# Optimization experiments

Hardware: AMD Instinct MI355X
Metric: run time of the kernel (lower is better)

The kernel has to match this reference:

```python
import jax, jax.numpy as jnp
import numpy as np

B, H, W, P = 2, 224, 224, 256


def setup_inputs() -> dict:
    key = jax.random.key(0)
    ks = jax.random.split(key, 7)
    x = jax.random.normal(ks[0], (B, 1, H, W), dtype=jnp.float32)
    offset_x1 = jax.random.uniform(ks[1], (P,), jnp.float32, -16.0, 16.0)
    offset_x2 = jax.random.uniform(ks[2], (P,), jnp.float32, -16.0, 16.0)
    offset_y1 = jax.random.uniform(ks[3], (P,), jnp.float32, -16.0, 16.0)
    offset_y2 = jax.random.uniform(ks[4], (P,), jnp.float32, -16.0, 16.0)
    radii = jax.random.randint(ks[5], (P,), 1, 4).astype(jnp.int32)  # {1,2,3}
    thresholds = jax.random.normal(ks[6], (P,), dtype=jnp.float32) * 0.1
    return {
        'x': x,
        'offset_x1': offset_x1, 'offset_x2': offset_x2,
        'offset_y1': offset_y1, 'offset_y2': offset_y2,
        'radii': radii, 'thresholds': thresholds,
        'max_radius': 3,
    }


def reference(x, offset_x1, offset_x2, offset_y1, offset_y2, radii, thresholds, max_radius):
    Bb, _, Hh, Ww = x.shape
    r = int(max_radius)
    dtype = x.dtype
    # replicate-padded integral image, zero-padded by 1 on top/left -> [B, Hp+1, Wp+1]
    xp = jnp.pad(x, ((0, 0), (0, 0), (r, r), (r, r)), mode='edge')
    integral = jnp.cumsum(jnp.cumsum(xp, axis=2), axis=3)
    integral = jnp.pad(integral, ((0, 0), (0, 0), (1, 0), (1, 0)))[:, 0]

    base_y = jnp.arange(Hh, dtype=dtype)[None, :, None]   # [1,H,1]
    base_x = jnp.arange(Ww, dtype=dtype)[None, None, :]   # [1,1,W]
    rad = radii.astype(jnp.int32)[:, None, None]           # [P,1,1]
    area = ((2.0 * radii.astype(dtype) + 1.0) ** 2)[:, None, None]

    def box_mean(off_y, off_x):
        # clamped float centers, truncated to int (non-negative -> trunc == floor)
        cy = jnp.clip(base_y + off_y[:, None, None], 0.0, Hh - 1).astype(jnp.int32) + r
        cx = jnp.clip(base_x + off_x[:, None, None], 0.0, Ww - 1).astype(jnp.int32) + r
        y0, x0 = cy - rad, cx - rad
        y1, x1 = cy + rad + 1, cx + rad + 1
        g = lambda yi, xi: integral[:, yi, xi]  # gather -> [B,P,H,W]
        s = g(y1, x1) - g(y0, x1) - g(y1, x0) + g(y0, x0)
        return s / area

    diff = box_mean(offset_y1, offset_x1) - box_mean(offset_y2, offset_x2)
    # binarize=False: return centered differences
    return diff - thresholds[None, :, None, None].astype(diff.dtype)
```

## Files before the change

kernel.cpp:

```cpp
#include <hip/hip_runtime.h>

#define BN 2
#define HN 224
#define WN 224
#define PN 256
#define RN 3
#define IW 231
#define ISZ (IW * IW)
#define NPIX (HN * WN)

__global__ __launch_bounds__(256) void integral_rows_kernel(
    const float* __restrict__ x, float* __restrict__ I)
{
    const int wave = (blockIdx.x * 256 + threadIdx.x) >> 6;
    const int lane = threadIdx.x & 63;
    if (wave >= BN * IW) return;
    const int b = wave / IW, i = wave % IW;
    float* Ib = I + b * ISZ + i * IW;
    if (i == 0) {
        for (int j = lane; j < IW; j += 64) Ib[j] = 0.0f;
        return;
    }
    int yy = i - 1 - RN;
    yy = yy < 0 ? 0 : (yy > HN - 1 ? HN - 1 : yy);
    const float* xr = x + b * HN * WN + yy * WN;

    float carry = 0.0f;
#pragma unroll
    for (int c = 0; c < 4; ++c) {
        const int j = c * 64 + lane;
        float v = 0.0f;
        if (j >= 1 && j < IW) {
            int xx = j - 1 - RN;
            xx = xx < 0 ? 0 : (xx > WN - 1 ? WN - 1 : xx);
            v = xr[xx];
        }
#pragma unroll
        for (int d = 1; d < 64; d <<= 1) {
            float n = __shfl_up(v, d, 64);
            if (lane >= d) v += n;
        }
        v += carry;
        if (j < IW) Ib[j] = v;
        carry = __shfl(v, 63, 64);
    }
}

__global__ __launch_bounds__(256) void integral_cols_kernel(float* __restrict__ I)
{
    const int t = blockIdx.x * 256 + threadIdx.x;
    if (t >= BN * IW) return;
    const int b = t / IW, j = t % IW;
    float* Ib = I + b * ISZ;
    float acc = 0.0f;
#pragma unroll 11
    for (int i = 1; i < IW; ++i) {
        acc += Ib[i * IW + j];
        Ib[i * IW + j] = acc;
    }
}

__global__ __launch_bounds__(256) void box_mean_kernel(
    const float* __restrict__ I, float* __restrict__ BM)
{
    const int xt = blockIdx.x;
    const int zb = blockIdx.z;
    const int r_idx = zb >> 1, b = zb & 1;
    const int rad = r_idx + 1;
    const float inv_area = 1.0f / (float)((2 * rad + 1) * (2 * rad + 1));
    const int x = xt * 64 + threadIdx.x;
    const int xc = x < WN ? x : WN - 1;
    const int y = blockIdx.y * 4 + threadIdx.y;

    const float* Ib = I + b * ISZ;
    const int y0 = y + RN - rad, y1 = y + RN + rad + 1;
    const int x0 = xc + RN - rad, x1 = xc + RN + rad + 1;
    const float* rlo = Ib + y0 * IW;
    const float* rhi = Ib + y1 * IW;
    const float s = rhi[x1] - rlo[x1] - rhi[x0] + rlo[x0];
    if (x < WN)
        BM[(size_t)zb * NPIX + y * WN + x] = s * inv_area;
}

__global__ __launch_bounds__(256) void bad_main_kernel(
    const float* __restrict__ BM,
    const float* __restrict__ ox1, const float* __restrict__ ox2,
    const float* __restrict__ oy1, const float* __restrict__ oy2,
    const int*   __restrict__ radii, const float* __restrict__ thr,
    float* __restrict__ out)
{
    const int p  = blockIdx.y;
    const int b  = blockIdx.z;
    const int xt = blockIdx.x & 3;
    const int yt = blockIdx.x >> 2;
    const int x  = xt * 64 + threadIdx.x;
    const int y0 = yt * (HN / 2) + threadIdx.y;

    const float offx1 = ox1[p], offx2 = ox2[p];
    const float offy1 = oy1[p], offy2 = oy2[p];
    const int   rad   = radii[p];
    const float t     = thr[p];

    const float* map = BM + (size_t)((rad - 1) * BN + b) * NPIX;

    const float fx = (float)x;
    const int vx1 = (int)fminf(fmaxf(fx + offx1, 0.0f), (float)(WN - 1));
    const int vx2 = (int)fminf(fmaxf(fx + offx2, 0.0f), (float)(WN - 1));

    const bool xok = (x < WN);
    float* outp = out + (size_t)(b * PN + p) * NPIX + (size_t)y0 * WN;

#pragma unroll 4
    for (int i = 0; i < HN / 2; i += 4) {
        const float fy = (float)(y0 + i);
        const int cy1 = __builtin_amdgcn_readfirstlane(
                            (int)fminf(fmaxf(fy + offy1, 0.0f), (float)(HN - 1)));
        const int cy2 = __builtin_amdgcn_readfirstlane(
                            (int)fminf(fmaxf(fy + offy2, 0.0f), (float)(HN - 1)));
        const float v1 = map[cy1 * WN + vx1];
        const float v2 = map[cy2 * WN + vx2];
        if (xok) outp[i * WN + x] = v1 - v2 - t;
    }
}

extern "C" void kernel_launch(void* const* d_in, const int* in_sizes, int n_in,
                              void* d_out, int out_size, void* d_ws, size_t ws_size,
                              hipStream_t stream)
{
    const float* x    = (const float*)d_in[0];
    const float* ox1  = (const float*)d_in[1];
    const float* ox2  = (const float*)d_in[2];
    const float* oy1  = (const float*)d_in[3];
    const float* oy2  = (const float*)d_in[4];
    const int*   rad  = (const int*)d_in[5];
    const float* thr  = (const float*)d_in[6];

    float* I  = (float*)d_ws;
    float* BM = I + BN * ISZ;
    float* out = (float*)d_out;

    hipLaunchKernelGGL(integral_rows_kernel, dim3((BN * IW * 64 + 255) / 256), dim3(256), 0, stream, x, I);
    hipLaunchKernelGGL(integral_cols_kernel, dim3((BN * IW + 255) / 256), dim3(256), 0, stream, I);
    hipLaunchKernelGGL(box_mean_kernel,      dim3(4, HN / 4, 6), dim3(64, 4, 1), 0, stream, I, BM);
    hipLaunchKernelGGL(bad_main_kernel,      dim3(8, PN, BN), dim3(64, 4, 1), 0, stream,
                       BM, ox1, ox2, oy1, oy2, rad, thr, out);
}
```

Before: 148.5 us.

## Replace integral-image pipeline with direct box-sum kernel for box means

Removes the two integral-image kernels (row scan and column scan) and computes each radius's box mean directly from the clamped input with templated unrolled sums. This eliminates two launches and the serial column-scan kernel that used few threads. The cost is more loads per output (up to 49 for radius 3), which mostly hit cache. Summation order differs from the integral-difference approach, so numerics change slightly and could even be more accurate.

```diff
diff --git a/kernel.cpp b/kernel.cpp
--- a/kernel.cpp
+++ b/kernel.cpp
@@ -4,82 +4,46 @@
 #define HN 224
 #define WN 224
 #define PN 256
-#define RN 3
-#define IW 231
-#define ISZ (IW * IW)
 #define NPIX (HN * WN)
 
-__global__ __launch_bounds__(256) void integral_rows_kernel(
-    const float* __restrict__ x, float* __restrict__ I)
+template<int RAD>
+__device__ __forceinline__ float box_sum(const float* __restrict__ xb, int y, int xc)
 {
-    const int wave = (blockIdx.x * 256 + threadIdx.x) >> 6;
-    const int lane = threadIdx.x & 63;
-    if (wave >= BN * IW) return;
-    const int b = wave / IW, i = wave % IW;
-    float* Ib = I + b * ISZ + i * IW;
-    if (i == 0) {
-        for (int j = lane; j < IW; j += 64) Ib[j] = 0.0f;
-        return;
+    int xs[2 * RAD + 1];
+#pragma unroll
+    for (int dx = -RAD; dx <= RAD; ++dx) {
+        int xx = xc + dx;
+        xs[dx + RAD] = xx < 0 ? 0 : (xx > WN - 1 ? WN - 1 : xx);
     }
-    int yy = i - 1 - RN;
-    yy = yy < 0 ? 0 : (yy > HN - 1 ? HN - 1 : yy);
-    const float* xr = x + b * HN * WN + yy * WN;
-
-    float carry = 0.0f;
+    float s = 0.0f;
 #pragma unroll
-    for (int c = 0; c < 4; ++c) {
-        const int j = c * 64 + lane;
-        float v = 0.0f;
-        if (j >= 1 && j < IW) {
-            int xx = j - 1 - RN;
-            xx = xx < 0 ? 0 : (xx > WN - 1 ? WN - 1 : xx);
-            v = xr[xx];
-        }
+    for (int dy = -RAD; dy <= RAD; ++dy) {
+        int yy = y + dy;
+        yy = yy < 0 ? 0 : (yy > HN - 1 ? HN - 1 : yy);
+        const float* row = xb + yy * WN;
 #pragma unroll
-        for (int d = 1; d < 64; d <<= 1) {
-            float n = __shfl_up(v, d, 64);
-            if (lane >= d) v += n;
-        }
-        v += carry;
-        if (j < IW) Ib[j] = v;
-        carry = __shfl(v, 63, 64);
+        for (int k = 0; k < 2 * RAD + 1; ++k) s += row[xs[k]];
     }
+    return s;
 }
 
-__global__ __launch_bounds__(256) void integral_cols_kernel(float* __restrict__ I)
+__global__ __launch_bounds__(256) void box_mean_direct_kernel(
+    const float* __restrict__ x, float* __restrict__ BM)
 {
-    const int t = blockIdx.x * 256 + threadIdx.x;
-    if (t >= BN * IW) return;
-    const int b = t / IW, j = t % IW;
-    float* Ib = I + b * ISZ;
-    float acc = 0.0f;
-#pragma unroll 11
-    for (int i = 1; i < IW; ++i) {
-        acc += Ib[i * IW + j];
-        Ib[i * IW + j] = acc;
-    }
-}
-
-__global__ __launch_bounds__(256) void box_mean_kernel(
-    const float* __restrict__ I, float* __restrict__ BM)
-{
-    const int xt = blockIdx.x;
     const int zb = blockIdx.z;
     const int r_idx = zb >> 1, b = zb & 1;
-    const int rad = r_idx + 1;
-    const float inv_area = 1.0f / (float)((2 * rad + 1) * (2 * rad + 1));
-    const int x = xt * 64 + threadIdx.x;
-    const int xc = x < WN ? x : WN - 1;
-    const int y = blockIdx.y * 4 + threadIdx.y;
+    const int xi = blockIdx.x * 64 + threadIdx.x;
+    const int y  = blockIdx.y * 4 + threadIdx.y;
+    const int xc = xi < WN ? xi : WN - 1;
 
-    const float* Ib = I + b * ISZ;
-    const int y0 = y + RN - rad, y1 = y + RN + rad + 1;
-    const int x0 = xc + RN - rad, x1 = xc + RN + rad + 1;
-    const float* rlo = Ib + y0 * IW;
-    const float* rhi = Ib + y1 * IW;
-    const float s = rhi[x1] - rlo[x1] - rhi[x0] + rlo[x0];
-    if (x < WN)
-        BM[(size_t)zb * NPIX + y * WN + x] = s * inv_area;
+    const float* xb = x + b * NPIX;
+    float s;
+    if (r_idx == 0)      s = box_sum<1>(xb, y, xc) * (1.0f / 9.0f);
+    else if (r_idx == 1) s = box_sum<2>(xb, y, xc) * (1.0f / 25.0f);
+    else                 s = box_sum<3>(xb, y, xc) * (1.0f / 49.0f);
+
+    if (xi < WN)
+        BM[(size_t)zb * NPIX + y * WN + xi] = s;
 }
 
 __global__ __launch_bounds__(256) void bad_main_kernel(
@@ -135,13 +99,10 @@
     const int*   rad  = (const int*)d_in[5];
     const float* thr  = (const float*)d_in[6];
 
-    float* I  = (float*)d_ws;
-    float* BM = I + BN * ISZ;
+    float* BM  = (float*)d_ws;
     float* out = (float*)d_out;
 
-    hipLaunchKernelGGL(integral_rows_kernel, dim3((BN * IW * 64 + 255) / 256), dim3(256), 0, stream, x, I);
-    hipLaunchKernelGGL(integral_cols_kernel, dim3((BN * IW + 255) / 256), dim3(256), 0, stream, I);
-    hipLaunchKernelGGL(box_mean_kernel,      dim3(4, HN / 4, 6), dim3(64, 4, 1), 0, stream, I, BM);
-    hipLaunchKernelGGL(bad_main_kernel,      dim3(8, PN, BN), dim3(64, 4, 1), 0, stream,
+    hipLaunchKernelGGL(box_mean_direct_kernel, dim3(4, HN / 4, 6), dim3(64, 4, 1), 0, stream, x, BM);
+    hipLaunchKernelGGL(bad_main_kernel,        dim3(8, PN, BN), dim3(64, 4, 1), 0, stream,
                        BM, ox1, ox2, oy1, oy2, rad, thr, out);
 }
```

Result: faster. 133.9 us (-9.8%).
